# Kernel optimization log

Measured on AMD Instinct MI355X. Metric: run time of the kernel, lower is better.

The kernel has to match this reference:

```python
import jax, jax.numpy as jnp
import numpy as np

B, S, D = 1, 4096, 1024
H, Dh = 16, 64
F = 4096  # mlp_factor * D
EPS = 1e-6


def _ln(x, scale, bias=None):
    m = jnp.mean(x, axis=-1, keepdims=True)
    v = jnp.var(x, axis=-1, keepdims=True)
    y = (x - m) * jax.lax.rsqrt(v + EPS) * scale
    return y + bias if bias is not None else y


def setup_inputs() -> dict:
    key = jax.random.key(0)
    ks = jax.random.split(key, 10)
    lecun = lambda k, shape, fan_in: (jax.random.normal(k, shape, jnp.float32) * (fan_in ** -0.5))
    inp = {
        "x": jax.random.normal(ks[0], (B, S, D), jnp.float32),
        # causal mask, broadcastable to [B, H, S, S]
        "mask": jnp.tril(jnp.ones((S, S), bool))[None, None],
        # PreNorm (TPNorm -> LayerNorm)
        "ln_scale": jnp.ones((D,), jnp.float32),
        "ln_bias": jnp.zeros((D,), jnp.float32),
        # MLP input projection
        "w_in": lecun(ks[1], (D, F), D),
        "b_in": jnp.zeros((F,), jnp.float32),
        # QKV projection
        "wq": lecun(ks[2], (D, H, Dh), D),
        "bq": jnp.zeros((H, Dh), jnp.float32),
        "wk": lecun(ks[3], (D, H, Dh), D),
        "bk": jnp.zeros((H, Dh), jnp.float32),
        "wv": lecun(ks[4], (D, H, Dh), D),
        "bv": jnp.zeros((H, Dh), jnp.float32),
        # qk-norm scales (normalize_qk=True)
        "qn_scale": jnp.ones((Dh,), jnp.float32),
        "kn_scale": jnp.ones((Dh,), jnp.float32),
        # MLP output projection
        "w_mo": lecun(ks[5], (F, D), F),
        "b_mo": jnp.zeros((D,), jnp.float32),
        # Attention output projection
        "w_ao": lecun(ks[6], (H * Dh, D), H * Dh),
        "b_ao": jnp.zeros((D,), jnp.float32),
    }
    return inp


def reference(x, mask, ln_scale, ln_bias, w_in, b_in, wq, bq, wk, bk, wv, bv,
              qn_scale, kn_scale, w_mo, b_mo, w_ao, b_ao):
    residual = x
    xn = _ln(x, ln_scale, ln_bias)

    # fused QKV + MLP-input projections (QKVMLPDenseParallel)
    h = jax.nn.gelu(jnp.einsum("bsd,df->bsf", xn, w_in) + b_in)  # [B,S,F]
    q = jnp.einsum("bsd,dhk->bshk", xn, wq) + bq  # [B,S,H,Dh]
    k = jnp.einsum("bsd,dhk->bshk", xn, wk) + bk
    v = jnp.einsum("bsd,dhk->bshk", xn, wv) + bv
    # normalize_qk: per-head LayerNorm (no bias) on q, k
    q = _ln(q, qn_scale)
    k = _ln(k, kn_scale)

    # dot-product attention
    scores = jnp.einsum("bqhd,bkhd->bhqk", q, k) / np.sqrt(Dh).astype(np.float32)
    scores = jnp.where(mask, scores, jnp.finfo(scores.dtype).min)
    attn = jax.nn.softmax(scores, axis=-1)
    o = jnp.einsum("bhqk,bkhd->bqhd", attn, v)  # [B,S,H,Dh]

    # fused attention-out + MLP-out projections (AttnMLPOutParallel)
    mlp_out = jnp.einsum("bsf,fd->bsd", h, w_mo) + b_mo
    attn_out = jnp.einsum("bse,ed->bsd", o.reshape(B, S, H * Dh), w_ao) + b_ao

    # dropout deterministic (train=False); residual add
    return residual + mlp_out + attn_out
```

## Files before the change

### kernel.cpp

```cpp
#include <hip/hip_runtime.h>
#include <hip/hip_fp16.h>

typedef _Float16 half8 __attribute__((ext_vector_type(8)));
typedef float floatx4 __attribute__((ext_vector_type(4)));

constexpr int kS = 4096;
constexpr int kD = 1024;
constexpr int kH = 16;
constexpr int kDh = 64;
constexpr int kF = 4096;
constexpr int kNQKV = kF + 3 * kD;
constexpr int kKOut = kF + kD;

__device__ __forceinline__ void async_ld16(const void* g, void* l) {
  __builtin_amdgcn_global_load_lds(
      (const __attribute__((address_space(1))) void*)g,
      (__attribute__((address_space(3))) void*)l, 16, 0, 0);
}

__global__ __launch_bounds__(256) void wtrans_kernel(
    const float* __restrict__ src, _Float16* __restrict__ dst,
    int N, int dldk, int noff, int koff) {
  __shared__ float t[32][33];
  const int tid = threadIdx.x;
  const int n0 = blockIdx.x * 32, k0 = blockIdx.y * 32;
#pragma unroll
  for (int i = 0; i < 4; ++i) {
    const int kl = (tid >> 5) + i * 8, nl = tid & 31;
    t[kl][nl] = src[(size_t)(k0 + kl) * N + n0 + nl];
  }
  __syncthreads();
#pragma unroll
  for (int i = 0; i < 4; ++i) {
    const int nl = (tid >> 5) + i * 8, kl = tid & 31;
    dst[(size_t)(noff + n0 + nl) * dldk + koff + k0 + kl] = (_Float16)t[kl][nl];
  }
}

__global__ __launch_bounds__(256) void htrans_kernel(
    const _Float16* __restrict__ src, _Float16* __restrict__ dst, int R, int C) {
  __shared__ _Float16 t[32][34];
  const int tid = threadIdx.x;
  const int c0 = blockIdx.x * 32, r0 = blockIdx.y * 32;
#pragma unroll
  for (int i = 0; i < 4; ++i) {
    const int rl = (tid >> 5) + i * 8, cl = tid & 31;
    t[rl][cl] = src[(size_t)(r0 + rl) * C + c0 + cl];
  }
  __syncthreads();
#pragma unroll
  for (int i = 0; i < 4; ++i) {
    const int cl = (tid >> 5) + i * 8, rl = tid & 31;
    dst[(size_t)(c0 + cl) * R + r0 + rl] = t[rl][cl];
  }
}

__global__ __launch_bounds__(256) void biasprep_kernel(
    const float* b_in, const float* bq, const float* bk, const float* bv,
    const float* b_mo, const float* b_ao, float* bcat, float* bsum) {
  const int i = blockIdx.x * 256 + threadIdx.x;
  if (i < kF) bcat[i] = b_in[i];
  else if (i < kF + kD) bcat[i] = bq[i - kF];
  else if (i < kF + 2 * kD) bcat[i] = bk[i - kF - kD];
  else if (i < kNQKV) bcat[i] = bv[i - kF - 2 * kD];
  else if (i < kNQKV + kD) bsum[i - kNQKV] = b_mo[i - kNQKV] + b_ao[i - kNQKV];
}

__global__ __launch_bounds__(256) void ln_kernel(
    const float* __restrict__ x, const float* __restrict__ scale,
    const float* __restrict__ bias, _Float16* __restrict__ xn) {
  const int row = blockIdx.x;
  const int tid = threadIdx.x;
  const float* xr = x + (size_t)row * kD;
  float v[4];
  float s = 0.f, sq = 0.f;
#pragma unroll
  for (int i = 0; i < 4; ++i) {
    v[i] = xr[tid + 256 * i];
    s += v[i];
    sq += v[i] * v[i];
  }
  for (int off = 32; off; off >>= 1) {
    s += __shfl_xor(s, off);
    sq += __shfl_xor(sq, off);
  }
  __shared__ float red[8];
  const int wv = tid >> 6;
  if ((tid & 63) == 0) { red[wv] = s; red[wv + 4] = sq; }
  __syncthreads();
  s = red[0] + red[1] + red[2] + red[3];
  sq = red[4] + red[5] + red[6] + red[7];
  const float mean = s * (1.0f / kD);
  const float var = sq * (1.0f / kD) - mean * mean;
  const float rstd = rsqrtf(var + 1e-6f);
#pragma unroll
  for (int i = 0; i < 4; ++i) {
    int d = tid + 256 * i;
    xn[(size_t)row * kD + d] = (_Float16)((v[i] - mean) * rstd * scale[d] + bias[d]);
  }
}

__global__ __launch_bounds__(256) void qknorm_kernel(
    _Float16* __restrict__ t, const float* __restrict__ scale, float smul) {
  const int row = (blockIdx.x << 2) + (threadIdx.x >> 6);
  const int lane = threadIdx.x & 63;
  _Float16* tr = t + (size_t)row * kDh;
  const float val = (float)tr[lane];
  float s = val;
  for (int off = 32; off; off >>= 1) s += __shfl_xor(s, off);
  const float mean = s * (1.0f / kDh);
  const float dv = val - mean;
  float sq = dv * dv;
  for (int off = 32; off; off >>= 1) sq += __shfl_xor(sq, off);
  const float rstd = rsqrtf(sq * (1.0f / kDh) + 1e-6f);
  tr[lane] = (_Float16)(dv * rstd * scale[lane] * smul);
}

__global__ __launch_bounds__(256) void gemm_qkvin(
    const _Float16* __restrict__ A, const _Float16* __restrict__ Bp,
    const float* __restrict__ bcat, _Float16* __restrict__ ho,
    _Float16* __restrict__ q, _Float16* __restrict__ k, _Float16* __restrict__ v) {
  __shared__ alignas(16) _Float16 Ts[16 * 512];
  _Float16* As = Ts;
  _Float16* Bs = Ts + 8 * 512;

  const int tid = threadIdx.x;
  const int lane = tid & 63;
  const int wave = tid >> 6;
  const int wm = (wave >> 1) * 64;
  const int wn = (wave & 1) * 64;
  const int m0 = blockIdx.x * 128;
  const int n0 = blockIdx.y * 128;
  const int lrow = lane & 15;
  const int quad = lane >> 4;

  floatx4 acc[4][4] = {};

  for (int k0 = 0; k0 < kD; k0 += 32) {
    __syncthreads();
#pragma unroll
    for (int i = 0; i < 4; ++i) {
      const int chunk = wave * 4 + i;
      const int r = ((chunk & 7) << 4) + (lane >> 2);
      const int csrc = ((lane & 3) ^ ((r >> 1) & 3)) << 3;
      const _Float16* src = (chunk < 8)
          ? A + (size_t)(m0 + r) * kD + k0 + csrc
          : Bp + (size_t)(n0 + r) * kD + k0 + csrc;
      async_ld16(src, Ts + chunk * 512);
    }
    __syncthreads();

    half8 af[4], bf[4];
#pragma unroll
    for (int i = 0; i < 4; ++i) {
      const int ra = wm + i * 16 + lrow;
      const int rb = wn + i * 16 + lrow;
      af[i] = *reinterpret_cast<const half8*>(&As[ra * 32 + ((quad ^ ((ra >> 1) & 3)) << 3)]);
      bf[i] = *reinterpret_cast<const half8*>(&Bs[rb * 32 + ((quad ^ ((rb >> 1) & 3)) << 3)]);
    }
#pragma unroll
    for (int i = 0; i < 4; ++i)
#pragma unroll
      for (int j = 0; j < 4; ++j)
        acc[i][j] = __builtin_amdgcn_mfma_f32_16x16x32_f16(af[i], bf[j], acc[i][j], 0, 0, 0);
  }

#pragma unroll
  for (int i = 0; i < 4; ++i) {
    const int gm = m0 + wm + i * 16 + quad * 4;
#pragma unroll
    for (int j = 0; j < 4; ++j) {
      const int gn = n0 + wn + j * 16 + lrow;
      const float bn = bcat[gn];
#pragma unroll
      for (int r = 0; r < 4; ++r) {
        float vv = acc[i][j][r] + bn;
        if (gn < kF) {
          const float xv = vv;
          vv = 0.5f * xv * (1.0f + tanhf(0.7978845608028654f * (xv + 0.044715f * xv * xv * xv)));
          ho[(size_t)(gm + r) * kKOut + gn] = (_Float16)vv;
        } else {
          const int reg = gn - kF;
          _Float16* dst = (reg < kD) ? q : (reg < 2 * kD) ? k : v;
          dst[(size_t)(gm + r) * kD + (reg & (kD - 1))] = (_Float16)vv;
        }
      }
    }
  }
}

__global__ __launch_bounds__(256) void gemm_out(
    const _Float16* __restrict__ A, const _Float16* __restrict__ Bp,
    const float* __restrict__ bsum, const float* __restrict__ x,
    float* __restrict__ out) {
  __shared__ alignas(16) _Float16 Ts[12 * 512];
  _Float16* As = Ts;
  _Float16* Bs = Ts + 8 * 512;

  const int tid = threadIdx.x;
  const int lane = tid & 63;
  const int wave = tid >> 6;
  const int m0 = blockIdx.x * 128;
  const int n0 = blockIdx.y * 64;
  const int lrow = lane & 15;
  const int quad = lane >> 4;

  floatx4 acc[2][4] = {};

  for (int k0 = 0; k0 < kKOut; k0 += 32) {
    __syncthreads();
#pragma unroll
    for (int i = 0; i < 3; ++i) {
      const int chunk = wave * 3 + i;
      const int rl = (lane >> 2);
      const int csrc = ((lane & 3) ^ (((chunk < 8 ? ((chunk & 7) << 4) + rl
                                                 : ((chunk - 8) << 4) + rl) >> 1) & 3)) << 3;
      const _Float16* src;
      if (chunk < 8) {
        const int r = ((chunk & 7) << 4) + rl;
        src = A + (size_t)(m0 + r) * kKOut + k0 + csrc;
      } else {
        const int r = ((chunk - 8) << 4) + rl;
        src = Bp + (size_t)(n0 + r) * kKOut + k0 + csrc;
      }
      async_ld16(src, Ts + chunk * 512);
    }
    __syncthreads();

    half8 af[2], bf[4];
#pragma unroll
    for (int i = 0; i < 2; ++i) {
      const int ra = wave * 32 + i * 16 + lrow;
      af[i] = *reinterpret_cast<const half8*>(&As[ra * 32 + ((quad ^ ((ra >> 1) & 3)) << 3)]);
    }
#pragma unroll
    for (int j = 0; j < 4; ++j) {
      const int rb = j * 16 + lrow;
      bf[j] = *reinterpret_cast<const half8*>(&Bs[rb * 32 + ((quad ^ ((rb >> 1) & 3)) << 3)]);
    }
#pragma unroll
    for (int i = 0; i < 2; ++i)
#pragma unroll
      for (int j = 0; j < 4; ++j)
        acc[i][j] = __builtin_amdgcn_mfma_f32_16x16x32_f16(af[i], bf[j], acc[i][j], 0, 0, 0);
  }

#pragma unroll
  for (int i = 0; i < 2; ++i) {
    const int gm = m0 + wave * 32 + i * 16 + quad * 4;
#pragma unroll
    for (int j = 0; j < 4; ++j) {
      const int gn = n0 + j * 16 + lrow;
      const float bn = bsum[gn];
#pragma unroll
      for (int r = 0; r < 4; ++r) {
        const size_t idx = (size_t)(gm + r) * kD + gn;
        out[idx] = x[idx] + bn + acc[i][j][r];
      }
    }
  }
}

__global__ __launch_bounds__(256) void fattn_kernel(
    const _Float16* __restrict__ Q, const _Float16* __restrict__ K,
    const _Float16* __restrict__ Vt, _Float16* __restrict__ ho) {
  __shared__ alignas(16) _Float16 Qs[64 * 64];
  __shared__ alignas(16) _Float16 Ks[64 * 64];
  __shared__ alignas(16) _Float16 Vs[64 * 64];
  __shared__ alignas(16) _Float16 Ps[64 * 72];

  const int tid = threadIdx.x;
  const int lane = tid & 63;
  const int wave = tid >> 6;
  const int lrow = lane & 15;
  const int quad = lane >> 4;
  const int h = blockIdx.y;
  const int pair = blockIdx.x;

  const int rs = lane >> 3;
  const int cs = lane & 7;

  for (int pass = 0; pass < 2; ++pass) {
    const int qtile = pass ? (63 - pair) : pair;
    const int qbase = qtile * 64;

    __syncthreads();
    {
#pragma unroll
      for (int i = 0; i < 2; ++i) {
        const int chunk = wave * 2 + i;
        const int r = chunk * 8 + rs;
        async_ld16(Q + (size_t)(qbase + r) * kD + h * kDh + ((cs ^ (r & 7)) << 3),
                   Qs + chunk * 512);
      }
    }
    __syncthreads();

    half8 qf[2];
#pragma unroll
    for (int kt = 0; kt < 2; ++kt)
      qf[kt] = *reinterpret_cast<const half8*>(
          &Qs[(wave * 16 + lrow) * 64 + (((kt * 4 + quad) ^ (lrow & 7)) << 3)]);

    float mst[4], lst[4];
    floatx4 oacc[4] = {};
#pragma unroll
    for (int r = 0; r < 4; ++r) { mst[r] = -1e30f; lst[r] = 0.f; }

    const int qw = qbase + wave * 16;

    for (int t = 0; t <= qtile; ++t) {
      const int k0 = t * 64;
      __syncthreads();
      {
#pragma unroll
        for (int i = 0; i < 4; ++i) {
          const int id = wave * 4 + i;
          if (id < 8) {
            const int r = id * 8 + rs;
            async_ld16(K + (size_t)(k0 + r) * kD + h * kDh + ((cs ^ (r & 7)) << 3),
                       Ks + id * 512);
          } else {
            const int c = id - 8;
            const int r = c * 8 + rs;
            async_ld16(Vt + (size_t)(h * kDh + r) * kS + k0 + ((cs ^ (r & 7)) << 3),
                       Vs + c * 512);
          }
        }
      }
      __syncthreads();

      const bool diag = (t == qtile);

      floatx4 sacc[4] = {};
#pragma unroll
      for (int jt = 0; jt < 4; ++jt) {
        if (diag && jt > wave) continue;
#pragma unroll
        for (int kt = 0; kt < 2; ++kt) {
          const int rb = jt * 16 + lrow;
          half8 bfk = *reinterpret_cast<const half8*>(
              &Ks[rb * 64 + (((kt * 4 + quad) ^ (lrow & 7)) << 3)]);
          sacc[jt] = __builtin_amdgcn_mfma_f32_16x16x32_f16(qf[kt], bfk, sacc[jt], 0, 0, 0);
        }
      }

      if (diag) {
#pragma unroll
        for (int jt = 0; jt < 4; ++jt) {
          const int kg = k0 + jt * 16 + lrow;
#pragma unroll
          for (int r = 0; r < 4; ++r)
            if (kg > qw + quad * 4 + r) sacc[jt][r] = -1e30f;
        }
      }

#pragma unroll
      for (int r = 0; r < 4; ++r) {
        float mx = fmaxf(fmaxf(sacc[0][r], sacc[1][r]), fmaxf(sacc[2][r], sacc[3][r]));
#pragma unroll
        for (int off = 8; off; off >>= 1) mx = fmaxf(mx, __shfl_xor(mx, off));
        const float mnew = fmaxf(mst[r], mx);
        const float alpha = __expf(mst[r] - mnew);
        mst[r] = mnew;
        float rsum = 0.f;
#pragma unroll
        for (int jt = 0; jt < 4; ++jt) {
          const float p = __expf(sacc[jt][r] - mnew);
          sacc[jt][r] = p;
          rsum += p;
        }
#pragma unroll
        for (int off = 8; off; off >>= 1) rsum += __shfl_xor(rsum, off);
        lst[r] = lst[r] * alpha + rsum;
#pragma unroll
        for (int jt = 0; jt < 4; ++jt) oacc[jt][r] *= alpha;
      }

#pragma unroll
      for (int jt = 0; jt < 4; ++jt)
#pragma unroll
        for (int r = 0; r < 4; ++r)
          Ps[(wave * 16 + quad * 4 + r) * 72 + jt * 16 + lrow] = (_Float16)sacc[jt][r];

      const int ktmax = (diag && wave < 2) ? 1 : 2;
      for (int kt = 0; kt < ktmax; ++kt) {
        half8 pf = *reinterpret_cast<const half8*>(
            &Ps[(wave * 16 + lrow) * 72 + (kt * 4 + quad) * 8]);
#pragma unroll
        for (int jt = 0; jt < 4; ++jt) {
          const int rb = jt * 16 + lrow;
          half8 vf = *reinterpret_cast<const half8*>(
              &Vs[rb * 64 + (((kt * 4 + quad) ^ (lrow & 7)) << 3)]);
          oacc[jt] = __builtin_amdgcn_mfma_f32_16x16x32_f16(pf, vf, oacc[jt], 0, 0, 0);
        }
      }
    }

#pragma unroll
    for (int jt = 0; jt < 4; ++jt) {
      const int d = jt * 16 + lrow;
#pragma unroll
      for (int r = 0; r < 4; ++r)
        ho[(size_t)(qw + quad * 4 + r) * kKOut + kF + h * kDh + d] =
            (_Float16)(oacc[jt][r] / lst[r]);
    }
  }
}

extern "C" void kernel_launch(void* const* d_in, const int* in_sizes, int n_in,
                              void* d_out, int out_size, void* d_ws, size_t ws_size,
                              hipStream_t stream) {
  const float* x        = (const float*)d_in[0];
  const float* ln_scale = (const float*)d_in[2];
  const float* ln_bias  = (const float*)d_in[3];
  const float* w_in     = (const float*)d_in[4];
  const float* b_in     = (const float*)d_in[5];
  const float* wq       = (const float*)d_in[6];
  const float* bq       = (const float*)d_in[7];
  const float* wk       = (const float*)d_in[8];
  const float* bk       = (const float*)d_in[9];
  const float* wv       = (const float*)d_in[10];
  const float* bv       = (const float*)d_in[11];
  const float* qn_scale = (const float*)d_in[12];
  const float* kn_scale = (const float*)d_in[13];
  const float* w_mo     = (const float*)d_in[14];
  const float* b_mo     = (const float*)d_in[15];
  const float* w_ao     = (const float*)d_in[16];
  const float* b_ao     = (const float*)d_in[17];
  float* out = (float*)d_out;

  char* ws = (char*)d_ws;
  size_t off = 0;
  auto alloc = [&](size_t bytes) { char* p = ws + off; off += bytes; return p; };
  _Float16* xn    = (_Float16*)alloc((size_t)kS * kD * 2);
  _Float16* Wqkv  = (_Float16*)alloc((size_t)kNQKV * kD * 2);
  _Float16* Wout  = (_Float16*)alloc((size_t)kD * kKOut * 2);
  float*    bcat  = (float*)alloc((size_t)kNQKV * 4);
  float*    bsum  = (float*)alloc((size_t)kD * 4);
  _Float16* ho    = (_Float16*)alloc((size_t)kS * kKOut * 2);
  _Float16* q_h   = (_Float16*)alloc((size_t)kS * kD * 2);
  _Float16* k_h   = (_Float16*)alloc((size_t)kS * kD * 2);
  _Float16* v_h   = (_Float16*)alloc((size_t)kS * kD * 2);
  _Float16* v_t   = (_Float16*)alloc((size_t)kS * kD * 2);

  wtrans_kernel<<<dim3(kF / 32, kD / 32), 256, 0, stream>>>(w_in, Wqkv, kF, kD, 0, 0);
  wtrans_kernel<<<dim3(kD / 32, kD / 32), 256, 0, stream>>>(wq, Wqkv, kD, kD, kF, 0);
  wtrans_kernel<<<dim3(kD / 32, kD / 32), 256, 0, stream>>>(wk, Wqkv, kD, kD, kF + kD, 0);
  wtrans_kernel<<<dim3(kD / 32, kD / 32), 256, 0, stream>>>(wv, Wqkv, kD, kD, kF + 2 * kD, 0);
  wtrans_kernel<<<dim3(kD / 32, kF / 32), 256, 0, stream>>>(w_mo, Wout, kD, kKOut, 0, 0);
  wtrans_kernel<<<dim3(kD / 32, kD / 32), 256, 0, stream>>>(w_ao, Wout, kD, kKOut, 0, kF);

  biasprep_kernel<<<(kNQKV + kD + 255) / 256, 256, 0, stream>>>(
      b_in, bq, bk, bv, b_mo, b_ao, bcat, bsum);

  ln_kernel<<<kS, 256, 0, stream>>>(x, ln_scale, ln_bias, xn);

  gemm_qkvin<<<dim3(kS / 128, kNQKV / 128), 256, 0, stream>>>(
      xn, Wqkv, bcat, ho, q_h, k_h, v_h);

  qknorm_kernel<<<kS * kH / 4, 256, 0, stream>>>(q_h, qn_scale, 0.125f);
  qknorm_kernel<<<kS * kH / 4, 256, 0, stream>>>(k_h, kn_scale, 1.0f);

  htrans_kernel<<<dim3(kD / 32, kS / 32), 256, 0, stream>>>(v_h, v_t, kS, kD);

  fattn_kernel<<<dim3(32, kH), 256, 0, stream>>>(q_h, k_h, v_t, ho);

  gemm_out<<<dim3(kS / 128, kD / 64), 256, 0, stream>>>(ho, Wout, bsum, x, out);
}
```

Baseline: 523.6 us.

## Split attention and output GEMM over K with atomics, fixed-offset softmax, fast GELU

Flash attention now runs two key-splits per query tile. It uses a fixed exponent offset instead of an online max, because qk-norm bounds the scores, and the log2e scale is folded into the q normalization. Partial O and L are accumulated with float atomics, and a separate kernel normalizes the result into ho. The output GEMM moves to 128x128 tiles with a split-K of 2 and atomicAdd into an output that is pre-initialized with x plus bias. GELU switches from tanhf to an exp2-based sigmoid form. Together these aim for more parallelism and fewer transcendental operations, at the cost of atomic traffic, extra launches, and numerical reliance on the bounded score range.

Result: faster. 494.5 us (-5.6%).

```diff
diff --git a/kernel.cpp b/kernel.cpp
--- a/kernel.cpp
+++ b/kernel.cpp
@@ -116,6 +116,12 @@
   tr[lane] = (_Float16)(dv * rstd * scale[lane] * smul);
 }
 
+__device__ __forceinline__ float fast_gelu(float xv) {
+  const float z = 0.7978845608028654f * (xv + 0.044715f * xv * xv * xv);
+  const float u = exp2f(fminf(2.885390081777927f * z, 80.0f));
+  return xv * u / (1.0f + u);
+}
+
 __global__ __launch_bounds__(256) void gemm_qkvin(
     const _Float16* __restrict__ A, const _Float16* __restrict__ Bp,
     const float* __restrict__ bcat, _Float16* __restrict__ ho,
@@ -176,9 +182,7 @@
       for (int r = 0; r < 4; ++r) {
         float vv = acc[i][j][r] + bn;
         if (gn < kF) {
-          const float xv = vv;
-          vv = 0.5f * xv * (1.0f + tanhf(0.7978845608028654f * (xv + 0.044715f * xv * xv * xv)));
-          ho[(size_t)(gm + r) * kKOut + gn] = (_Float16)vv;
+          ho[(size_t)(gm + r) * kKOut + gn] = (_Float16)fast_gelu(vv);
         } else {
           const int reg = gn - kF;
           _Float16* dst = (reg < kD) ? q : (reg < 2 * kD) ? k : v;
@@ -189,81 +193,84 @@
   }
 }
 
+__global__ __launch_bounds__(256) void initout_kernel(
+    const float* __restrict__ x, const float* __restrict__ bsum,
+    float* __restrict__ out) {
+  const int i = blockIdx.x * 256 + threadIdx.x;
+  out[i] = x[i] + bsum[i & (kD - 1)];
+}
+
 __global__ __launch_bounds__(256) void gemm_out(
     const _Float16* __restrict__ A, const _Float16* __restrict__ Bp,
-    const float* __restrict__ bsum, const float* __restrict__ x,
     float* __restrict__ out) {
-  __shared__ alignas(16) _Float16 Ts[12 * 512];
+  __shared__ alignas(16) _Float16 Ts[16 * 512];
   _Float16* As = Ts;
   _Float16* Bs = Ts + 8 * 512;
 
   const int tid = threadIdx.x;
   const int lane = tid & 63;
   const int wave = tid >> 6;
+  const int wm = (wave >> 1) * 64;
+  const int wn = (wave & 1) * 64;
   const int m0 = blockIdx.x * 128;
-  const int n0 = blockIdx.y * 64;
+  const int n0 = blockIdx.y * 128;
+  const int kbeg = blockIdx.z * (kKOut / 2);
   const int lrow = lane & 15;
   const int quad = lane >> 4;
 
-  floatx4 acc[2][4] = {};
-
-  for (int k0 = 0; k0 < kKOut; k0 += 32) {
-    __syncthreads();
-#pragma unroll
-    for (int i = 0; i < 3; ++i) {
-      const int chunk = wave * 3 + i;
-      const int rl = (lane >> 2);
-      const int csrc = ((lane & 3) ^ (((chunk < 8 ? ((chunk & 7) << 4) + rl
-                                                 : ((chunk - 8) << 4) + rl) >> 1) & 3)) << 3;
-      const _Float16* src;
-      if (chunk < 8) {
-        const int r = ((chunk & 7) << 4) + rl;
-        src = A + (size_t)(m0 + r) * kKOut + k0 + csrc;
-      } else {
-        const int r = ((chunk - 8) << 4) + rl;
-        src = Bp + (size_t)(n0 + r) * kKOut + k0 + csrc;
-      }
+  floatx4 acc[4][4] = {};
+
+  for (int k0 = kbeg; k0 < kbeg + kKOut / 2; k0 += 32) {
+    __syncthreads();
+#pragma unroll
+    for (int i = 0; i < 4; ++i) {
+      const int chunk = wave * 4 + i;
+      const int r = ((chunk & 7) << 4) + (lane >> 2);
+      const int csrc = ((lane & 3) ^ ((r >> 1) & 3)) << 3;
+      const _Float16* src = (chunk < 8)
+          ? A + (size_t)(m0 + r) * kKOut + k0 + csrc
+          : Bp + (size_t)(n0 + r) * kKOut + k0 + csrc;
       async_ld16(src, Ts + chunk * 512);
     }
     __syncthreads();
 
-    half8 af[2], bf[4];
-#pragma unroll
-    for (int i = 0; i < 2; ++i) {
-      const int ra = wave * 32 + i * 16 + lrow;
+    half8 af[4], bf[4];
+#pragma unroll
+    for (int i = 0; i < 4; ++i) {
+      const int ra = wm + i * 16 + lrow;
+      const int rb = wn + i * 16 + lrow;
       af[i] = *reinterpret_cast<const half8*>(&As[ra * 32 + ((quad ^ ((ra >> 1) & 3)) << 3)]);
-    }
-#pragma unroll
-    for (int j = 0; j < 4; ++j) {
-      const int rb = j * 16 + lrow;
-      bf[j] = *reinterpret_cast<const half8*>(&Bs[rb * 32 + ((quad ^ ((rb >> 1) & 3)) << 3)]);
-    }
-#pragma unroll
-    for (int i = 0; i < 2; ++i)
+      bf[i] = *reinterpret_cast<const half8*>(&Bs[rb * 32 + ((quad ^ ((rb >> 1) & 3)) << 3)]);
+    }
+#pragma unroll
+    for (int i = 0; i < 4; ++i)
 #pragma unroll
       for (int j = 0; j < 4; ++j)
         acc[i][j] = __builtin_amdgcn_mfma_f32_16x16x32_f16(af[i], bf[j], acc[i][j], 0, 0, 0);
   }
 
 #pragma unroll
-  for (int i = 0; i < 2; ++i) {
-    const int gm = m0 + wave * 32 + i * 16 + quad * 4;
+  for (int i = 0; i < 4; ++i) {
+    const int gm = m0 + wm + i * 16 + quad * 4;
 #pragma unroll
     for (int j = 0; j < 4; ++j) {
-      const int gn = n0 + j * 16 + lrow;
-      const float bn = bsum[gn];
-#pragma unroll
-      for (int r = 0; r < 4; ++r) {
-        const size_t idx = (size_t)(gm + r) * kD + gn;
-        out[idx] = x[idx] + bn + acc[i][j][r];
-      }
-    }
-  }
+      const int gn = n0 + wn + j * 16 + lrow;
+#pragma unroll
+      for (int r = 0; r < 4; ++r)
+        atomicAdd(out + (size_t)(gm + r) * kD + gn, acc[i][j][r]);
+    }
+  }
+}
+
+__global__ __launch_bounds__(256) void zeroacc_kernel(float* __restrict__ p, int n) {
+  const int i = blockIdx.x * 256 + threadIdx.x;
+  if (i < n) p[i] = 0.f;
 }
 
 __global__ __launch_bounds__(256) void fattn_kernel(
     const _Float16* __restrict__ Q, const _Float16* __restrict__ K,
-    const _Float16* __restrict__ Vt, _Float16* __restrict__ ho) {
+    const _Float16* __restrict__ Vt, float* __restrict__ Oacc,
+    float* __restrict__ Lacc) {
   __shared__ alignas(16) _Float16 Qs[64 * 64];
   __shared__ alignas(16) _Float16 Ks[64 * 64];
   __shared__ alignas(16) _Float16 Vs[64 * 64];
@@ -276,23 +283,23 @@
   const int quad = lane >> 4;
   const int h = blockIdx.y;
   const int pair = blockIdx.x;
+  const int split = blockIdx.z;
 
   const int rs = lane >> 3;
   const int cs = lane & 7;
+  constexpr float kOff = 11.5415603f;
 
   for (int pass = 0; pass < 2; ++pass) {
     const int qtile = pass ? (63 - pair) : pair;
     const int qbase = qtile * 64;
 
     __syncthreads();
-    {
-#pragma unroll
-      for (int i = 0; i < 2; ++i) {
-        const int chunk = wave * 2 + i;
-        const int r = chunk * 8 + rs;
-        async_ld16(Q + (size_t)(qbase + r) * kD + h * kDh + ((cs ^ (r & 7)) << 3),
-                   Qs + chunk * 512);
-      }
+#pragma unroll
+    for (int i = 0; i < 2; ++i) {
+      const int chunk = wave * 2 + i;
+      const int r = chunk * 8 + rs;
+      async_ld16(Q + (size_t)(qbase + r) * kD + h * kDh + ((cs ^ (r & 7)) << 3),
+                 Qs + chunk * 512);
     }
     __syncthreads();
 
@@ -302,30 +309,25 @@
       qf[kt] = *reinterpret_cast<const half8*>(
           &Qs[(wave * 16 + lrow) * 64 + (((kt * 4 + quad) ^ (lrow & 7)) << 3)]);
 
-    float mst[4], lst[4];
+    float lst[4] = {0.f, 0.f, 0.f, 0.f};
     floatx4 oacc[4] = {};
-#pragma unroll
-    for (int r = 0; r < 4; ++r) { mst[r] = -1e30f; lst[r] = 0.f; }
-
     const int qw = qbase + wave * 16;
 
-    for (int t = 0; t <= qtile; ++t) {
+    for (int t = split; t <= qtile; t += 2) {
       const int k0 = t * 64;
       __syncthreads();
-      {
-#pragma unroll
-        for (int i = 0; i < 4; ++i) {
-          const int id = wave * 4 + i;
-          if (id < 8) {
-            const int r = id * 8 + rs;
-            async_ld16(K + (size_t)(k0 + r) * kD + h * kDh + ((cs ^ (r & 7)) << 3),
-                       Ks + id * 512);
-          } else {
-            const int c = id - 8;
-            const int r = c * 8 + rs;
-            async_ld16(Vt + (size_t)(h * kDh + r) * kS + k0 + ((cs ^ (r & 7)) << 3),
-                       Vs + c * 512);
-          }
+#pragma unroll
+      for (int i = 0; i < 4; ++i) {
+        const int id = wave * 4 + i;
+        if (id < 8) {
+          const int r = id * 8 + rs;
+          async_ld16(K + (size_t)(k0 + r) * kD + h * kDh + ((cs ^ (r & 7)) << 3),
+                     Ks + id * 512);
+        } else {
+          const int c = id - 8;
+          const int r = c * 8 + rs;
+          async_ld16(Vt + (size_t)(h * kDh + r) * kS + k0 + ((cs ^ (r & 7)) << 3),
+                     Vs + c * 512);
         }
       }
       __syncthreads();
@@ -356,26 +358,13 @@
       }
 
 #pragma unroll
-      for (int r = 0; r < 4; ++r) {
-        float mx = fmaxf(fmaxf(sacc[0][r], sacc[1][r]), fmaxf(sacc[2][r], sacc[3][r]));
-#pragma unroll
-        for (int off = 8; off; off >>= 1) mx = fmaxf(mx, __shfl_xor(mx, off));
-        const float mnew = fmaxf(mst[r], mx);
-        const float alpha = __expf(mst[r] - mnew);
-        mst[r] = mnew;
-        float rsum = 0.f;
-#pragma unroll
-        for (int jt = 0; jt < 4; ++jt) {
-          const float p = __expf(sacc[jt][r] - mnew);
+      for (int jt = 0; jt < 4; ++jt)
+#pragma unroll
+        for (int r = 0; r < 4; ++r) {
+          const float p = exp2f(sacc[jt][r] - kOff);
           sacc[jt][r] = p;
-          rsum += p;
-        }
-#pragma unroll
-        for (int off = 8; off; off >>= 1) rsum += __shfl_xor(rsum, off);
-        lst[r] = lst[r] * alpha + rsum;
-#pragma unroll
-        for (int jt = 0; jt < 4; ++jt) oacc[jt][r] *= alpha;
-      }
+          lst[r] += p;
+        }
 
 #pragma unroll
       for (int jt = 0; jt < 4; ++jt)
@@ -398,14 +387,28 @@
     }
 
 #pragma unroll
-    for (int jt = 0; jt < 4; ++jt) {
-      const int d = jt * 16 + lrow;
-#pragma unroll
-      for (int r = 0; r < 4; ++r)
-        ho[(size_t)(qw + quad * 4 + r) * kKOut + kF + h * kDh + d] =
-            (_Float16)(oacc[jt][r] / lst[r]);
-    }
-  }
+    for (int r = 0; r < 4; ++r) {
+#pragma unroll
+      for (int off = 8; off; off >>= 1) lst[r] += __shfl_xor(lst[r], off);
+    }
+#pragma unroll
+    for (int r = 0; r < 4; ++r) {
+      const int qg = qw + quad * 4 + r;
+      if (lrow == 0) atomicAdd(Lacc + qg * kH + h, lst[r]);
+#pragma unroll
+      for (int jt = 0; jt < 4; ++jt)
+        atomicAdd(Oacc + ((size_t)qg * kH + h) * kDh + jt * 16 + lrow, oacc[jt][r]);
+    }
+  }
+}
+
+__global__ __launch_bounds__(256) void norm_kernel(
+    const float* __restrict__ Oacc, const float* __restrict__ Lacc,
+    _Float16* __restrict__ ho) {
+  const int idx = blockIdx.x * 256 + threadIdx.x;
+  const int q = idx >> 10, rem = idx & 1023;
+  const float l = Lacc[(q << 4) + (rem >> 6)];
+  ho[(size_t)q * kKOut + kF + rem] = (_Float16)(Oacc[idx] / l);
 }
 
 extern "C" void kernel_launch(void* const* d_in, const int* in_sizes, int n_in,
@@ -433,16 +436,19 @@
   char* ws = (char*)d_ws;
   size_t off = 0;
   auto alloc = [&](size_t bytes) { char* p = ws + off; off += bytes; return p; };
-  _Float16* xn    = (_Float16*)alloc((size_t)kS * kD * 2);
-  _Float16* Wqkv  = (_Float16*)alloc((size_t)kNQKV * kD * 2);
-  _Float16* Wout  = (_Float16*)alloc((size_t)kD * kKOut * 2);
-  float*    bcat  = (float*)alloc((size_t)kNQKV * 4);
-  float*    bsum  = (float*)alloc((size_t)kD * 4);
-  _Float16* ho    = (_Float16*)alloc((size_t)kS * kKOut * 2);
-  _Float16* q_h   = (_Float16*)alloc((size_t)kS * kD * 2);
-  _Float16* k_h   = (_Float16*)alloc((size_t)kS * kD * 2);
-  _Float16* v_h   = (_Float16*)alloc((size_t)kS * kD * 2);
-  _Float16* v_t   = (_Float16*)alloc((size_t)kS * kD * 2);
+  char* zone = (char*)alloc((size_t)kS * kD * 2 + (size_t)kNQKV * kD * 2);
+  _Float16* xn   = (_Float16*)zone;
+  _Float16* Wqkv = (_Float16*)(zone + (size_t)kS * kD * 2);
+  float* Oacc = (float*)zone;
+  float* Lacc = (float*)(zone + (size_t)kS * kD * 4);
+  _Float16* Wout = (_Float16*)alloc((size_t)kD * kKOut * 2);
+  float*    bcat = (float*)alloc((size_t)kNQKV * 4);
+  float*    bsum = (float*)alloc((size_t)kD * 4);
+  _Float16* ho   = (_Float16*)alloc((size_t)kS * kKOut * 2);
+  _Float16* q_h  = (_Float16*)alloc((size_t)kS * kD * 2);
+  _Float16* k_h  = (_Float16*)alloc((size_t)kS * kD * 2);
+  _Float16* v_h  = (_Float16*)alloc((size_t)kS * kD * 2);
+  _Float16* v_t  = (_Float16*)alloc((size_t)kS * kD * 2);
 
   wtrans_kernel<<<dim3(kF / 32, kD / 32), 256, 0, stream>>>(w_in, Wqkv, kF, kD, 0, 0);
   wtrans_kernel<<<dim3(kD / 32, kD / 32), 256, 0, stream>>>(wq, Wqkv, kD, kD, kF, 0);
@@ -459,12 +465,18 @@
   gemm_qkvin<<<dim3(kS / 128, kNQKV / 128), 256, 0, stream>>>(
       xn, Wqkv, bcat, ho, q_h, k_h, v_h);
 
-  qknorm_kernel<<<kS * kH / 4, 256, 0, stream>>>(q_h, qn_scale, 0.125f);
+  qknorm_kernel<<<kS * kH / 4, 256, 0, stream>>>(q_h, qn_scale, 0.18033688f);
   qknorm_kernel<<<kS * kH / 4, 256, 0, stream>>>(k_h, kn_scale, 1.0f);
 
   htrans_kernel<<<dim3(kD / 32, kS / 32), 256, 0, stream>>>(v_h, v_t, kS, kD);
 
-  fattn_kernel<<<dim3(32, kH), 256, 0, stream>>>(q_h, k_h, v_t, ho);
-
-  gemm_out<<<dim3(kS / 128, kD / 64), 256, 0, stream>>>(ho, Wout, bsum, x, out);
-}
+  zeroacc_kernel<<<(kS * kD + kS * kH + 255) / 256, 256, 0, stream>>>(
+      Oacc, kS * kD + kS * kH);
+
+  fattn_kernel<<<dim3(32, kH, 2), 256, 0, stream>>>(q_h, k_h, v_t, Oacc, Lacc);
+
+  norm_kernel<<<kS * kD / 256, 256, 0, stream>>>(Oacc, Lacc, ho);
+
+  initout_kernel<<<kS * kD / 256, 256, 0, stream>>>(x, bsum, out);
+  gemm_out<<<dim3(kS / 128, kD / 128, 2), 256, 0, stream>>>(ho, Wout, out);
+}
```
